# Kernel optimization log

Measured on AMD Instinct MI355X. Metric: run time of the kernel, lower is better.

## Reference

```python
import jax, jax.numpy as jnp
import numpy as np

B, N, M = 2048, 4096, 4096


def setup_inputs() -> dict:
    key = jax.random.key(0)
    kt, kv, kr = jax.random.split(key, 3)
    # sorted abscissae per sample (interp1d assumes monotone t)
    t = jnp.sort(jax.random.uniform(kt, (B, N), dtype=jnp.float32), axis=-1)
    v = jax.random.normal(kv, (B, N), dtype=jnp.float32)
    # queries slightly outside [0,1] to exercise the extrapolation clamp
    r = jax.random.uniform(kr, (B, M), minval=-0.05, maxval=1.05, dtype=jnp.float32)
    return {"t": t, "v": v, "r": r}


def _interp1(t, v, r):
    # t: [N] sorted, v: [N], r: [M]
    idx = jnp.clip(jnp.searchsorted(t, r, side='right'), 1, t.shape[0] - 1)
    t0 = t[idx - 1]
    t1 = t[idx]
    v0 = v[idx - 1]
    v1 = v[idx]
    denom = jnp.where(t1 == t0, jnp.float32(1.0), t1 - t0)
    out = v0 + (r - t0) / denom * (v1 - v0)
    # scipy fill_value=(v[0], v[-1]) with bounds_error=False: clamp extrapolation
    out = jnp.where(r < t[0], v[0], out)
    out = jnp.where(r > t[-1], v[-1], out)
    return out


def reference(t, v, r):
    # batched 1D linear interpolation with clamped extrapolation -> [B, M]
    return jax.vmap(_interp1)(t, v, r)
```

## Files before the change

### kernel.cpp

```cpp
#include <hip/hip_runtime.h>
#include <float.h>

constexpr int B = 2048;
constexpr int N = 4096;
constexpr int M = 4096;
constexpr int K = 4088;
constexpr int T = 512;

__global__ __launch_bounds__(T, 8) void interp_kernel(
    const float* __restrict__ t,
    const float* __restrict__ v,
    const float* __restrict__ r,
    float* __restrict__ out) {
    __shared__ __align__(16) float st[N + 4];
    __shared__ __align__(16) float sv[N];
    __shared__ unsigned short lut[K];

    const int b = blockIdx.x;
    const float* tb = t + (size_t)b * N;
    const float* vb = v + (size_t)b * N;
    const float* rb = r + (size_t)b * M;
    float* ob = out + (size_t)b * M;

    const float4* r4 = (const float4*)rb;
    const int ia = threadIdx.x;
    const int ib = ia + T;
    const float4 qa = r4[ia];
    const float4 qb = r4[ib];

    for (int i = threadIdx.x; i < N / 4; i += T) {
        ((float4*)st)[i] = ((const float4*)tb)[i];
        ((float4*)sv)[i] = ((const float4*)vb)[i];
    }
    if (threadIdx.x == 0) { st[N] = FLT_MAX; st[N + 1] = FLT_MAX; }
    for (int k = threadIdx.x; k < K; k += T) lut[k] = (unsigned short)N;
    __syncthreads();

    for (int j = threadIdx.x; j < N; j += T) {
        const float tj = st[j];
        int khi = (int)(tj * (float)K);
        if (khi > K - 1) khi = K - 1;
        const int klo = (j > 0) ? (int)(st[j - 1] * (float)K) + 1 : 0;
        for (int k = klo; k <= khi; ++k) lut[k] = (unsigned short)j;
    }
    __syncthreads();

    const float tfirst = st[0];
    const float vfirst = sv[0];
    const float tlast = st[N - 1];
    const float vlast = sv[N - 1];

    float q[8] = {qa.x, qa.y, qa.z, qa.w, qb.x, qb.y, qb.z, qb.w};
    int lo[8];

    #pragma unroll
    for (int j = 0; j < 8; ++j) {
        int k = (int)(q[j] * (float)K);
        k = k < 0 ? 0 : (k > K - 1 ? K - 1 : k);
        lo[j] = lut[k];
    }
    #pragma unroll
    for (int j = 0; j < 8; ++j) {
        lo[j] += (st[lo[j]] <= q[j]) ? 1 : 0;
        lo[j] += (st[lo[j]] <= q[j]) ? 1 : 0;
        while (st[lo[j]] <= q[j]) ++lo[j];
    }
    float o[8];
    #pragma unroll
    for (int j = 0; j < 8; ++j) {
        const int idx = lo[j] < 1 ? 1 : (lo[j] > N - 1 ? N - 1 : lo[j]);
        const float t0 = st[idx - 1];
        const float t1 = st[idx];
        const float v0 = sv[idx - 1];
        const float v1 = sv[idx];
        const float d = t1 - t0;
        const float rden = __builtin_amdgcn_rcpf(d == 0.0f ? 1.0f : d);
        float oo = v0 + (q[j] - t0) * rden * (v1 - v0);
        oo = (q[j] < tfirst) ? vfirst : oo;
        oo = (q[j] > tlast) ? vlast : oo;
        o[j] = oo;
    }
    float4* o4 = (float4*)ob;
    o4[ia] = make_float4(o[0], o[1], o[2], o[3]);
    o4[ib] = make_float4(o[4], o[5], o[6], o[7]);
}

extern "C" void kernel_launch(void* const* d_in, const int* in_sizes, int n_in,
                              void* d_out, int out_size, void* d_ws, size_t ws_size,
                              hipStream_t stream) {
    const float* t = (const float*)d_in[0];
    const float* v = (const float*)d_in[1];
    const float* r = (const float*)d_in[2];
    float* out = (float*)d_out;
    interp_kernel<<<B, T, 0, stream>>>(t, v, r, out);
}
```

Baseline: 135.7 us.

## Process two batch rows per block with register prefetch of next row

Each block now handles two batch rows in sequence. The next row's t and v are loaded into registers while the current row's LUT is built and its queries are answered, so global loads overlap compute. The LUT fill also switches to 32-bit stores. In exchange the grid is half as large, which reduces parallelism and adds extra barriers between rows.

```diff
diff --git a/kernel.cpp b/kernel.cpp
--- a/kernel.cpp
+++ b/kernel.cpp
@@ -6,6 +6,8 @@
 constexpr int M = 4096;
 constexpr int K = 4088;
 constexpr int T = 512;
+constexpr int BPB = 2;
+constexpr int GRID = B / BPB;
 
 __global__ __launch_bounds__(T, 8) void interp_kernel(
     const float* __restrict__ t,
@@ -16,73 +18,91 @@
     __shared__ __align__(16) float sv[N];
     __shared__ unsigned short lut[K];
 
-    const int b = blockIdx.x;
-    const float* tb = t + (size_t)b * N;
-    const float* vb = v + (size_t)b * N;
-    const float* rb = r + (size_t)b * M;
-    float* ob = out + (size_t)b * M;
+    const int tid = threadIdx.x;
+    const int b0 = blockIdx.x * BPB;
 
-    const float4* r4 = (const float4*)rb;
-    const int ia = threadIdx.x;
-    const int ib = ia + T;
-    const float4 qa = r4[ia];
-    const float4 qb = r4[ib];
-
-    for (int i = threadIdx.x; i < N / 4; i += T) {
-        ((float4*)st)[i] = ((const float4*)tb)[i];
-        ((float4*)sv)[i] = ((const float4*)vb)[i];
+    float4 pt0, pt1, pv0, pv1;
+    {
+        const float4* tb4 = (const float4*)(t + (size_t)b0 * N);
+        const float4* vb4 = (const float4*)(v + (size_t)b0 * N);
+        pt0 = tb4[tid]; pt1 = tb4[tid + T];
+        pv0 = vb4[tid]; pv1 = vb4[tid + T];
     }
-    if (threadIdx.x == 0) { st[N] = FLT_MAX; st[N + 1] = FLT_MAX; }
-    for (int k = threadIdx.x; k < K; k += T) lut[k] = (unsigned short)N;
-    __syncthreads();
-
-    for (int j = threadIdx.x; j < N; j += T) {
-        const float tj = st[j];
-        int khi = (int)(tj * (float)K);
-        if (khi > K - 1) khi = K - 1;
-        const int klo = (j > 0) ? (int)(st[j - 1] * (float)K) + 1 : 0;
-        for (int k = klo; k <= khi; ++k) lut[k] = (unsigned short)j;
-    }
-    __syncthreads();
-
-    const float tfirst = st[0];
-    const float vfirst = sv[0];
-    const float tlast = st[N - 1];
-    const float vlast = sv[N - 1];
-
-    float q[8] = {qa.x, qa.y, qa.z, qa.w, qb.x, qb.y, qb.z, qb.w};
-    int lo[8];
 
     #pragma unroll
-    for (int j = 0; j < 8; ++j) {
-        int k = (int)(q[j] * (float)K);
-        k = k < 0 ? 0 : (k > K - 1 ? K - 1 : k);
-        lo[j] = lut[k];
+    for (int bb = 0; bb < BPB; ++bb) {
+        const int b = b0 + bb;
+        const float4* r4 = (const float4*)(r + (size_t)b * M);
+        float4* o4 = (float4*)(out + (size_t)b * M);
+
+        const float4 qa = r4[tid];
+        const float4 qb = r4[tid + T];
+
+        ((float4*)st)[tid]     = pt0;
+        ((float4*)st)[tid + T] = pt1;
+        ((float4*)sv)[tid]     = pv0;
+        ((float4*)sv)[tid + T] = pv1;
+        if (tid < 4) st[N + tid] = FLT_MAX;
+        for (int i = tid; i < K / 2; i += T)
+            ((unsigned int*)lut)[i] = ((unsigned)N << 16) | (unsigned)N;
+
+        if (bb + 1 < BPB) {
+            const float4* tb4 = (const float4*)(t + (size_t)(b + 1) * N);
+            const float4* vb4 = (const float4*)(v + (size_t)(b + 1) * N);
+            pt0 = tb4[tid]; pt1 = tb4[tid + T];
+            pv0 = vb4[tid]; pv1 = vb4[tid + T];
+        }
+        __syncthreads();
+
+        for (int j = tid; j < N; j += T) {
+            const float tj = st[j];
+            int khi = (int)(tj * (float)K);
+            if (khi > K - 1) khi = K - 1;
+            const int klo = (j > 0) ? (int)(st[j - 1] * (float)K) + 1 : 0;
+            for (int k = klo; k <= khi; ++k) lut[k] = (unsigned short)j;
+        }
+        __syncthreads();
+
+        const float tfirst = st[0];
+        const float vfirst = sv[0];
+        const float tlast = st[N - 1];
+        const float vlast = sv[N - 1];
+
+        float q[8] = {qa.x, qa.y, qa.z, qa.w, qb.x, qb.y, qb.z, qb.w};
+        int lo[8];
+
+        #pragma unroll
+        for (int j = 0; j < 8; ++j) {
+            int k = (int)(q[j] * (float)K);
+            k = k < 0 ? 0 : (k > K - 1 ? K - 1 : k);
+            lo[j] = lut[k];
+        }
+        #pragma unroll
+        for (int j = 0; j < 8; ++j) {
+            lo[j] += (st[lo[j]] <= q[j]) ? 1 : 0;
+            lo[j] += (st[lo[j]] <= q[j]) ? 1 : 0;
+            while (st[lo[j]] <= q[j]) ++lo[j];
+        }
+        float o[8];
+        #pragma unroll
+        for (int j = 0; j < 8; ++j) {
+            const int idx = lo[j] < 1 ? 1 : (lo[j] > N - 1 ? N - 1 : lo[j]);
+            const float t0 = st[idx - 1];
+            const float t1 = st[idx];
+            const float v0 = sv[idx - 1];
+            const float v1 = sv[idx];
+            const float d = t1 - t0;
+            const float rden = __builtin_amdgcn_rcpf(d == 0.0f ? 1.0f : d);
+            float oo = v0 + (q[j] - t0) * rden * (v1 - v0);
+            oo = (q[j] < tfirst) ? vfirst : oo;
+            oo = (q[j] > tlast) ? vlast : oo;
+            o[j] = oo;
+        }
+        o4[tid] = make_float4(o[0], o[1], o[2], o[3]);
+        o4[tid + T] = make_float4(o[4], o[5], o[6], o[7]);
+
+        if (bb + 1 < BPB) __syncthreads();
     }
-    #pragma unroll
-    for (int j = 0; j < 8; ++j) {
-        lo[j] += (st[lo[j]] <= q[j]) ? 1 : 0;
-        lo[j] += (st[lo[j]] <= q[j]) ? 1 : 0;
-        while (st[lo[j]] <= q[j]) ++lo[j];
-    }
-    float o[8];
-    #pragma unroll
-    for (int j = 0; j < 8; ++j) {
-        const int idx = lo[j] < 1 ? 1 : (lo[j] > N - 1 ? N - 1 : lo[j]);
-        const float t0 = st[idx - 1];
-        const float t1 = st[idx];
-        const float v0 = sv[idx - 1];
-        const float v1 = sv[idx];
-        const float d = t1 - t0;
-        const float rden = __builtin_amdgcn_rcpf(d == 0.0f ? 1.0f : d);
-        float oo = v0 + (q[j] - t0) * rden * (v1 - v0);
-        oo = (q[j] < tfirst) ? vfirst : oo;
-        oo = (q[j] > tlast) ? vlast : oo;
-        o[j] = oo;
-    }
-    float4* o4 = (float4*)ob;
-    o4[ia] = make_float4(o[0], o[1], o[2], o[3]);
-    o4[ib] = make_float4(o[4], o[5], o[6], o[7]);
 }
 
 extern "C" void kernel_launch(void* const* d_in, const int* in_sizes, int n_in,
@@ -92,5 +112,5 @@
     const float* v = (const float*)d_in[1];
     const float* r = (const float*)d_in[2];
     float* out = (float*)d_out;
-    interp_kernel<<<B, T, 0, stream>>>(t, v, r, out);
+    interp_kernel<<<GRID, T, 0, stream>>>(t, v, r, out);
 }
```

After: 144.7 us. 1.07x slower.

## Replace serial LDS probe chain with aligned 6-wide window load and count

Applied to the files above, without the earlier changes.

After the LUT lookup, each query now loads an aligned window of six t values with three float2 LDS reads. It counts how many are <= q to find the bracket, instead of doing dependent single-element probes. t0/t1 come from the registers through a select tree, so only v is reloaded. The LUT is initialized with 32-bit stores, K shrinks slightly and the sentinel padding grows. This trades dependent LDS latency for more registers and compares, and processes the 8 queries in two passes of 4 to limit register pressure.

```diff
diff --git a/kernel.cpp b/kernel.cpp
--- a/kernel.cpp
+++ b/kernel.cpp
@@ -4,39 +4,46 @@
 constexpr int B = 2048;
 constexpr int N = 4096;
 constexpr int M = 4096;
-constexpr int K = 4088;
+constexpr int K = 4080;
 constexpr int T = 512;
+
+__device__ __forceinline__ float sel6(const float* w, int m) {
+    const float x0 = (m & 1) ? w[1] : w[0];
+    const float x2 = (m & 1) ? w[3] : w[2];
+    const float x4 = (m & 1) ? w[5] : w[4];
+    const float y0 = (m & 2) ? x2 : x0;
+    return (m & 4) ? x4 : y0;
+}
 
 __global__ __launch_bounds__(T, 8) void interp_kernel(
     const float* __restrict__ t,
     const float* __restrict__ v,
     const float* __restrict__ r,
     float* __restrict__ out) {
-    __shared__ __align__(16) float st[N + 4];
+    __shared__ __align__(16) float st[N + 8];
     __shared__ __align__(16) float sv[N];
     __shared__ unsigned short lut[K];
 
+    const int tid = threadIdx.x;
     const int b = blockIdx.x;
     const float* tb = t + (size_t)b * N;
     const float* vb = v + (size_t)b * N;
-    const float* rb = r + (size_t)b * M;
-    float* ob = out + (size_t)b * M;
+    const float4* r4 = (const float4*)(r + (size_t)b * M);
+    float4* o4 = (float4*)(out + (size_t)b * M);
 
-    const float4* r4 = (const float4*)rb;
-    const int ia = threadIdx.x;
-    const int ib = ia + T;
-    const float4 qa = r4[ia];
-    const float4 qb = r4[ib];
+    const float4 qa = r4[tid];
+    const float4 qb = r4[tid + T];
 
-    for (int i = threadIdx.x; i < N / 4; i += T) {
+    for (int i = tid; i < N / 4; i += T) {
         ((float4*)st)[i] = ((const float4*)tb)[i];
         ((float4*)sv)[i] = ((const float4*)vb)[i];
     }
-    if (threadIdx.x == 0) { st[N] = FLT_MAX; st[N + 1] = FLT_MAX; }
-    for (int k = threadIdx.x; k < K; k += T) lut[k] = (unsigned short)N;
+    if (tid < 8) st[N + tid] = FLT_MAX;
+    for (int i = tid; i < K / 2; i += T)
+        ((unsigned int*)lut)[i] = ((unsigned)N << 16) | (unsigned)N;
     __syncthreads();
 
-    for (int j = threadIdx.x; j < N; j += T) {
+    for (int j = tid; j < N; j += T) {
         const float tj = st[j];
         int khi = (int)(tj * (float)K);
         if (khi > K - 1) khi = K - 1;
@@ -50,39 +57,75 @@
     const float tlast = st[N - 1];
     const float vlast = sv[N - 1];
 
-    float q[8] = {qa.x, qa.y, qa.z, qa.w, qb.x, qb.y, qb.z, qb.w};
-    int lo[8];
+    float o[8];
+    const float4 qq[2] = {qa, qb};
+    #pragma unroll
+    for (int pass = 0; pass < 2; ++pass) {
+        float q[4] = {qq[pass].x, qq[pass].y, qq[pass].z, qq[pass].w};
+        int ja[4];
+        float w[4][6];
+        int cnt[4];
+        int idx[4];
 
-    #pragma unroll
-    for (int j = 0; j < 8; ++j) {
-        int k = (int)(q[j] * (float)K);
-        k = k < 0 ? 0 : (k > K - 1 ? K - 1 : k);
-        lo[j] = lut[k];
+        #pragma unroll
+        for (int j = 0; j < 4; ++j) {
+            int k = (int)(q[j] * (float)K);
+            k = k < 0 ? 0 : (k > K - 1 ? K - 1 : k);
+            int lo = lut[k];
+            lo = lo < 1 ? 1 : lo;
+            ja[j] = (lo - 1) & ~1;
+        }
+        #pragma unroll
+        for (int j = 0; j < 4; ++j) {
+            const float2* p = (const float2*)(st + ja[j]);
+            const float2 w01 = p[0];
+            const float2 w23 = p[1];
+            const float2 w45 = p[2];
+            w[j][0] = w01.x; w[j][1] = w01.y;
+            w[j][2] = w23.x; w[j][3] = w23.y;
+            w[j][4] = w45.x; w[j][5] = w45.y;
+        }
+        #pragma unroll
+        for (int j = 0; j < 4; ++j) {
+            int c = 0;
+            #pragma unroll
+            for (int s = 0; s < 6; ++s) c += (w[j][s] <= q[j]) ? 1 : 0;
+            int ix = ja[j] + c;
+            if (c == 6) {
+                int l = ja[j] + 6;
+                while (st[l] <= q[j]) ++l;
+                ix = l;
+                w[j][4] = st[ix - 1];
+                w[j][5] = st[ix];
+                c = 5;
+            }
+            cnt[j] = c;
+            idx[j] = ix;
+        }
+        float v0[4], v1[4];
+        #pragma unroll
+        for (int j = 0; j < 4; ++j) {
+            int ic = idx[j];
+            ic = ic < 1 ? 1 : (ic > N - 1 ? N - 1 : ic);
+            v0[j] = sv[ic - 1];
+            v1[j] = sv[ic];
+        }
+        #pragma unroll
+        for (int j = 0; j < 4; ++j) {
+            const int m1 = cnt[j];
+            const int m0 = m1 > 0 ? m1 - 1 : 0;
+            const float t1 = sel6(w[j], m1);
+            const float t0 = sel6(w[j], m0);
+            const float d = t1 - t0;
+            const float rden = __builtin_amdgcn_rcpf(d == 0.0f ? 1.0f : d);
+            float oo = v0[j] + (q[j] - t0) * rden * (v1[j] - v0[j]);
+            oo = (q[j] < tfirst) ? vfirst : oo;
+            oo = (q[j] > tlast) ? vlast : oo;
+            o[pass * 4 + j] = oo;
+        }
     }
-    #pragma unroll
-    for (int j = 0; j < 8; ++j) {
-        lo[j] += (st[lo[j]] <= q[j]) ? 1 : 0;
-        lo[j] += (st[lo[j]] <= q[j]) ? 1 : 0;
-        while (st[lo[j]] <= q[j]) ++lo[j];
-    }
-    float o[8];
-    #pragma unroll
-    for (int j = 0; j < 8; ++j) {
-        const int idx = lo[j] < 1 ? 1 : (lo[j] > N - 1 ? N - 1 : lo[j]);
-        const float t0 = st[idx - 1];
-        const float t1 = st[idx];
-        const float v0 = sv[idx - 1];
-        const float v1 = sv[idx];
-        const float d = t1 - t0;
-        const float rden = __builtin_amdgcn_rcpf(d == 0.0f ? 1.0f : d);
-        float oo = v0 + (q[j] - t0) * rden * (v1 - v0);
-        oo = (q[j] < tfirst) ? vfirst : oo;
-        oo = (q[j] > tlast) ? vlast : oo;
-        o[j] = oo;
-    }
-    float4* o4 = (float4*)ob;
-    o4[ia] = make_float4(o[0], o[1], o[2], o[3]);
-    o4[ib] = make_float4(o[4], o[5], o[6], o[7]);
+    o4[tid] = make_float4(o[0], o[1], o[2], o[3]);
+    o4[tid + T] = make_float4(o[4], o[5], o[6], o[7]);
 }
 
 extern "C" void kernel_launch(void* const* d_in, const int* in_sizes, int n_in,
```

Result: slower. 190.0 us (+40.0%).
